# Kernel optimization log

Measured on AMD Instinct MI355X. Metric: run time of the kernel, lower is better.

Reference implementation:

```python
import jax, jax.numpy as jnp
import numpy as np

N_NODES = 50000
N_EDGES = 800000
IN_F, HID, HEADS, OUT_F = 64, 64, 4, 64
NEG_SLOPE = 0.2


def _gat_conv(x, ei, W, a_src, a_dst, b, H, C):
    """PyG-style GATConv (eval mode, add_self_loops=True, concat=True).
    x: [N, F_in], ei: [2, E], W: [F_in, H*C], a_src/a_dst: [H, C], b: [H*C].
    """
    N = x.shape[0]
    h = (x @ W).reshape(N, H, C)                      # [N,H,C]
    asrc = jnp.einsum('nhc,hc->nh', h, a_src)         # [N,H]
    adst = jnp.einsum('nhc,hc->nh', h, a_dst)         # [N,H]
    src, dst = ei[0], ei[1]
    logits = jax.nn.leaky_relu(asrc[src] + adst[dst], NEG_SLOPE)  # [E,H]
    m = jax.ops.segment_max(logits, dst, num_segments=N)
    m = jnp.where(jnp.isfinite(m), m, 0.0)
    ex = jnp.exp(logits - m[dst])
    denom = jax.ops.segment_sum(ex, dst, num_segments=N)
    alpha = ex / (denom[dst] + 1e-16)                 # [E,H]
    msg = h[src] * alpha[:, :, None]                  # [E,H,C]
    out = jax.ops.segment_sum(msg, dst, num_segments=N)  # [N,H,C]
    return out.reshape(N, H * C) + b


def _add_self_loops(ei, n):
    loops = jnp.arange(n, dtype=ei.dtype)
    return jnp.concatenate([ei, jnp.stack([loops, loops])], axis=1)


def setup_inputs() -> dict:
    key = jax.random.key(0)
    ks = jax.random.split(key, 16)
    x = jax.random.normal(ks[0], (N_NODES, IN_F), dtype=jnp.float32)
    edge_index = jax.random.randint(ks[1], (2, N_EDGES), 0, N_NODES, dtype=jnp.int32)
    s = 0.1
    d = {'x': x, 'edge_index': edge_index}
    # layer 0: IN_F -> HID, HEADS heads
    d['W0'] = jax.random.normal(ks[2], (IN_F, HEADS * HID), jnp.float32) * s
    d['a_src0'] = jax.random.normal(ks[3], (HEADS, HID), jnp.float32) * s
    d['a_dst0'] = jax.random.normal(ks[4], (HEADS, HID), jnp.float32) * s
    d['b0'] = jnp.zeros((HEADS * HID,), jnp.float32)
    # layer 1: HEADS*HID -> HID, HEADS heads
    d['W1'] = jax.random.normal(ks[5], (HEADS * HID, HEADS * HID), jnp.float32) * s
    d['a_src1'] = jax.random.normal(ks[6], (HEADS, HID), jnp.float32) * s
    d['a_dst1'] = jax.random.normal(ks[7], (HEADS, HID), jnp.float32) * s
    d['b1'] = jnp.zeros((HEADS * HID,), jnp.float32)
    # layer 2: HEADS*HID -> OUT_F, 1 head
    d['W2'] = jax.random.normal(ks[8], (HEADS * HID, OUT_F), jnp.float32) * s
    d['a_src2'] = jax.random.normal(ks[9], (1, OUT_F), jnp.float32) * s
    d['a_dst2'] = jax.random.normal(ks[10], (1, OUT_F), jnp.float32) * s
    d['b2'] = jnp.zeros((OUT_F,), jnp.float32)
    return d


def reference(x, edge_index, W0, a_src0, a_dst0, b0, W1, a_src1, a_dst1, b1, W2, a_src2, a_dst2, b2):
    ei = _add_self_loops(edge_index, x.shape[0])
    h = _gat_conv(x, ei, W0, a_src0, a_dst0, b0, HEADS, HID)
    h = jax.nn.elu(h)  # dropout identity in eval
    h = _gat_conv(h, ei, W1, a_src1, a_dst1, b1, HEADS, HID)
    h = jax.nn.elu(h)
    out = _gat_conv(h, ei, W2, a_src2, a_dst2, b2, 1, OUT_F)
    return out
```

## Files before the change

### kernel.cpp

```cpp
#include <hip/hip_runtime.h>
#include <hip/hip_fp16.h>
#include <math.h>

#define NODES 50000
#define EDGES 800000
#define NB_SCAN ((NODES + 1023) / 1024)

typedef __attribute__((ext_vector_type(8))) _Float16 f16x8;
typedef __attribute__((ext_vector_type(4))) _Float16 f16x4;
typedef __attribute__((ext_vector_type(4))) float f32x4;

__device__ __forceinline__ float lrelu02(float x){ return x > 0.f ? x : 0.2f * x; }


__global__ __launch_bounds__(256) void gat_zero(int* __restrict__ p, int n){
  int i = blockIdx.x * 256 + threadIdx.x;
  if (i < n) p[i] = 0;
}

__global__ __launch_bounds__(256) void gat_hist(const int* __restrict__ ei, int* __restrict__ cnt){
  int e = blockIdx.x * 256 + threadIdx.x;
  if (e < EDGES) atomicAdd(&cnt[ei[EDGES + e]], 1);
}

__global__ __launch_bounds__(256) void gat_blocksum(const int* __restrict__ cnt, int* __restrict__ bsums){
  __shared__ int sd[256];
  int t = threadIdx.x, b = blockIdx.x;
  int base = b * 1024 + t * 4, s = 0;
  #pragma unroll
  for (int j = 0; j < 4; j++){ int i = base + j; if (i < NODES) s += cnt[i]; }
  sd[t] = s; __syncthreads();
  for (int o = 128; o > 0; o >>= 1){ if (t < o) sd[t] += sd[t + o]; __syncthreads(); }
  if (t == 0) bsums[b] = sd[0];
}

__global__ void gat_scan_bsums(int* bsums, int nb){
  if (threadIdx.x == 0 && blockIdx.x == 0){
    int run = 0;
    for (int i = 0; i < nb; i++){ int v = bsums[i]; bsums[i] = run; run += v; }
  }
}

__global__ __launch_bounds__(256) void gat_rowptr(int* __restrict__ cnt, const int* __restrict__ bsums,
                                                  int* __restrict__ row_ptr){
  __shared__ int sd[256];
  int t = threadIdx.x, b = blockIdx.x;
  int base = b * 1024 + t * 4;
  int c[4]; int s = 0;
  #pragma unroll
  for (int j = 0; j < 4; j++){
    int i = base + j;
    c[j] = (i < NODES) ? cnt[i] : 0;
    s += c[j];
    if (i < NODES) cnt[i] = 0;
  }
  sd[t] = s; __syncthreads();
  for (int o = 1; o < 256; o <<= 1){
    int v = (t >= o) ? sd[t - o] : 0;
    __syncthreads();
    if (t >= o) sd[t] += v;
    __syncthreads();
  }
  int off = bsums[b] + sd[t] - s;
  #pragma unroll
  for (int j = 0; j < 4; j++){
    int i = base + j;
    if (i < NODES){ row_ptr[i] = off; off += c[j]; }
  }
  if (b == 0 && t == 0) row_ptr[NODES] = EDGES;
}

__global__ __launch_bounds__(256) void gat_scatter(const int* __restrict__ ei, const int* __restrict__ row_ptr,
                                                    int* __restrict__ fill, int* __restrict__ col,
                                                    int* __restrict__ dstarr){
  int e = blockIdx.x * 256 + threadIdx.x;
  if (e < EDGES){
    int s = ei[e], d = ei[EDGES + e];
    int pos = row_ptr[d] + atomicAdd(&fill[d], 1);
    col[pos] = s;
    dstarr[pos] = d;
  }
}


__global__ __launch_bounds__(256) void gat_cvt_h(const float* __restrict__ src, _Float16* __restrict__ dst, int n4){
  int i = blockIdx.x * 256 + threadIdx.x;
  if (i < n4){
    float4 v = *(const float4*)(src + (size_t)i * 4);
    f16x4 h = { (_Float16)v.x, (_Float16)v.y, (_Float16)v.z, (_Float16)v.w };
    *(f16x4*)(dst + (size_t)i * 4) = h;
  }
}

__global__ __launch_bounds__(256) void gat_wt(const float* __restrict__ W, _Float16* __restrict__ Wt, int K, int N){
  int n = blockIdx.x * 256 + threadIdx.x;
  int k = blockIdx.y;
  if (n < N) Wt[(size_t)n * K + k] = (_Float16)W[(size_t)k * N + n];
}

__global__ __launch_bounds__(256) void gat_ws0(const float* __restrict__ W0, const float* __restrict__ a_src0,
                                               const float* __restrict__ a_dst0,
                                               float* __restrict__ ws, float* __restrict__ wd){
  int t = threadIdx.x;
  int h = t >> 6, c = t & 63;
  float s = 0.f, d = 0.f;
  for (int cc = 0; cc < 64; cc++){
    float w = W0[(size_t)c * 256 + h * 64 + cc];
    s += w * a_src0[h * 64 + cc];
    d += w * a_dst0[h * 64 + cc];
  }
  ws[h * 64 + c] = s;
  wd[h * 64 + c] = d;
}


template<int K, int N>
__global__ __launch_bounds__(256) void gat_gemm_mfma(const _Float16* __restrict__ A, const _Float16* __restrict__ Wt,
                                                      _Float16* __restrict__ C, int M){
  constexpr int NT = N / 64;
  constexpr int LDT = 40;
  __shared__ _Float16 As[64][LDT];
  __shared__ _Float16 Bs[N][LDT];

  int tid = threadIdx.x;
  int w = tid >> 6, l = tid & 63;
  int lg = l >> 4, lr = l & 15;
  int bm = blockIdx.x * 64;

  f32x4 acc[4][NT];
  #pragma unroll
  for (int m = 0; m < 4; m++)
    #pragma unroll
    for (int n = 0; n < NT; n++)
      acc[m][n] = (f32x4){0.f, 0.f, 0.f, 0.f};

  int ar = tid >> 2;
  int akc = (tid & 3) * 8;
  bool avalid = (bm + ar) < M;
  const _Float16* aptr = A + (size_t)(bm + ar) * K + akc;

  for (int k0 = 0; k0 < K; k0 += 32){
    float4 av = avalid ? *(const float4*)(aptr + k0) : make_float4(0.f, 0.f, 0.f, 0.f);
    __syncthreads();
    *(float4*)&As[ar][akc] = av;
    #pragma unroll
    for (int c = 0; c < N / 64; c++){
      int idx = c * 256 + tid;
      int n = idx >> 2, kc = (idx & 3) * 8;
      *(float4*)&Bs[n][kc] = *(const float4*)(Wt + (size_t)n * K + k0 + kc);
    }
    __syncthreads();

    f16x8 af[4], bf[NT];
    #pragma unroll
    for (int m = 0; m < 4; m++) af[m] = *(const f16x8*)&As[16 * m + lr][8 * lg];
    #pragma unroll
    for (int n = 0; n < NT; n++) bf[n] = *(const f16x8*)&Bs[w * (N / 4) + 16 * n + lr][8 * lg];
    #pragma unroll
    for (int m = 0; m < 4; m++)
      #pragma unroll
      for (int n = 0; n < NT; n++)
        acc[m][n] = __builtin_amdgcn_mfma_f32_16x16x32_f16(af[m], bf[n], acc[m][n], 0, 0, 0);
  }

  #pragma unroll
  for (int m = 0; m < 4; m++){
    #pragma unroll
    for (int j = 0; j < 4; j++){
      int row = bm + 16 * m + 4 * lg + j;
      if (row < M){
        #pragma unroll
        for (int n = 0; n < NT; n++)
          C[(size_t)row * N + w * (N / 4) + 16 * n + lr] = (_Float16)acc[m][n][j];
      }
    }
  }
}


__global__ __launch_bounds__(256) void gat_gemm_bd(const _Float16* __restrict__ A, const _Float16* __restrict__ Bt,
                                                    const float* __restrict__ bias, _Float16* __restrict__ C, int M){
  int tid = threadIdx.x;
  int w = tid >> 6, l = tid & 63;
  int lg = l >> 4, lr = l & 15;
  int bm = blockIdx.x * 64;

  f32x4 acc[4][4];
  #pragma unroll
  for (int m = 0; m < 4; m++)
    #pragma unroll
    for (int n = 0; n < 4; n++)
      acc[m][n] = (f32x4){0.f, 0.f, 0.f, 0.f};

  f16x8 zf = {};
  #pragma unroll
  for (int ks = 0; ks < 2; ks++){
    int koff = ks * 32;
    f16x8 af[4], bf[4];
    #pragma unroll
    for (int m = 0; m < 4; m++){
      int row = bm + 16 * m + lr;
      af[m] = (row < M) ? *(const f16x8*)(A + (size_t)row * 256 + w * 64 + koff + 8 * lg) : zf;
    }
    #pragma unroll
    for (int n = 0; n < 4; n++)
      bf[n] = *(const f16x8*)(Bt + (size_t)(w * 64 + 16 * n + lr) * 64 + koff + 8 * lg);
    #pragma unroll
    for (int m = 0; m < 4; m++)
      #pragma unroll
      for (int n = 0; n < 4; n++)
        acc[m][n] = __builtin_amdgcn_mfma_f32_16x16x32_f16(af[m], bf[n], acc[m][n], 0, 0, 0);
  }

  #pragma unroll
  for (int m = 0; m < 4; m++){
    #pragma unroll
    for (int j = 0; j < 4; j++){
      int row = bm + 16 * m + 4 * lg + j;
      if (row < M){
        #pragma unroll
        for (int n = 0; n < 4; n++){
          int cc = w * 64 + 16 * n + lr;
          float o = acc[m][n][j] + bias[cc];
          o = o > 0.f ? o : expm1f(o);
          C[(size_t)row * 256 + cc] = (_Float16)o;
        }
      }
    }
  }
}


__global__ __launch_bounds__(256) void gat_attn0(const _Float16* __restrict__ xh, const float* __restrict__ ws,
                                                  const float* __restrict__ wd,
                                                  float* __restrict__ asrc, float* __restrict__ adst, int N){
  int lane = threadIdx.x & 63;
  int wid = threadIdx.x >> 6;
  int n = blockIdx.x * 4 + wid;
  if (n >= N) return;
  float v = (float)xh[(size_t)n * 64 + lane];
  #pragma unroll
  for (int h = 0; h < 4; h++){
    float s1 = v * ws[h * 64 + lane];
    float s2 = v * wd[h * 64 + lane];
    #pragma unroll
    for (int o = 32; o > 0; o >>= 1){ s1 += __shfl_xor(s1, o); s2 += __shfl_xor(s2, o); }
    if (lane == 0){ asrc[n * 4 + h] = s1; adst[n * 4 + h] = s2; }
  }
}

__global__ __launch_bounds__(256) void gat_attn4(const _Float16* __restrict__ h, const float* __restrict__ a_src,
                                                  const float* __restrict__ a_dst,
                                                  float* __restrict__ asrc, float* __restrict__ adst, int N){
  int lane = threadIdx.x & 63;
  int wid = threadIdx.x >> 6;
  int n = blockIdx.x * 4 + wid;
  if (n >= N) return;
  int co = lane * 4;
  f16x4 hv = *(const f16x4*)(h + (size_t)n * 256 + co);
  float4 av = *(const float4*)&a_src[co];
  float4 dv = *(const float4*)&a_dst[co];
  float f0 = (float)hv[0], f1 = (float)hv[1], f2 = (float)hv[2], f3 = (float)hv[3];
  float s1 = f0 * av.x + f1 * av.y + f2 * av.z + f3 * av.w;
  float s2 = f0 * dv.x + f1 * dv.y + f2 * dv.z + f3 * dv.w;
  #pragma unroll
  for (int o = 8; o > 0; o >>= 1){ s1 += __shfl_xor(s1, o); s2 += __shfl_xor(s2, o); }
  if ((lane & 15) == 0){
    int q = lane >> 4;
    asrc[n * 4 + q] = s1;
    adst[n * 4 + q] = s2;
  }
}

__global__ __launch_bounds__(256) void gat_attn1(const _Float16* __restrict__ h, const float* __restrict__ a_src,
                                                  const float* __restrict__ a_dst,
                                                  float* __restrict__ asrc, float* __restrict__ adst, int N){
  int lane = threadIdx.x & 63;
  int wid = threadIdx.x >> 6;
  int n = blockIdx.x * 4 + wid;
  if (n >= N) return;
  float v = (float)h[(size_t)n * 64 + lane];
  float s1 = v * a_src[lane];
  float s2 = v * a_dst[lane];
  #pragma unroll
  for (int o = 32; o > 0; o >>= 1){ s1 += __shfl_xor(s1, o); s2 += __shfl_xor(s2, o); }
  if (lane == 0){ asrc[n] = s1; adst[n] = s2; }
}


__global__ __launch_bounds__(256) void gat_edge_exp0(const int* __restrict__ col, const int* __restrict__ dstarr,
                                                      const float* __restrict__ asrc, const float* __restrict__ adst,
                                                      float* __restrict__ exf){
  int i = blockIdx.x * 256 + threadIdx.x;
  if (i >= EDGES) return;
  int s = col[i], d = dstarr[i];
  float4 a = *(const float4*)&asrc[s * 4];
  float4 b = *(const float4*)&adst[d * 4];
  float4 r;
  r.x = __expf(lrelu02(a.x + b.x));
  r.y = __expf(lrelu02(a.y + b.y));
  r.z = __expf(lrelu02(a.z + b.z));
  r.w = __expf(lrelu02(a.w + b.w));
  *(float4*)&exf[(size_t)i * 4] = r;
}


__global__ __launch_bounds__(256) void gat_aggregate_in64(const _Float16* __restrict__ xh, const float* __restrict__ exf,
                                                           const float* __restrict__ asrc, const float* __restrict__ adst,
                                                           const int* __restrict__ row_ptr, const int* __restrict__ col,
                                                           _Float16* __restrict__ agg){
  int lane = threadIdx.x & 63;
  int wid = threadIdx.x >> 6;
  int d = blockIdx.x * 4 + wid;
  if (d >= NODES) return;

  float4 ad4 = *(const float4*)&adst[d * 4];
  float4 a4  = *(const float4*)&asrc[d * 4];
  float ex0 = __expf(lrelu02(a4.x + ad4.x));
  float ex1 = __expf(lrelu02(a4.y + ad4.y));
  float ex2 = __expf(lrelu02(a4.z + ad4.z));
  float ex3 = __expf(lrelu02(a4.w + ad4.w));
  float xv = (float)xh[(size_t)d * 64 + lane];
  float acc0 = ex0 * xv, acc1 = ex1 * xv, acc2 = ex2 * xv, acc3 = ex3 * xv;
  float den0 = ex0, den1 = ex1, den2 = ex2, den3 = ex3;

  int e0 = row_ptr[d], e1 = row_ptr[d + 1];
  const _Float16* xbase = xh + lane;
  int e = e0;
  for (; e + 4 <= e1; e += 4){
    int s0 = col[e], s1 = col[e + 1], s2 = col[e + 2], s3 = col[e + 3];
    float4 fA = *(const float4*)(exf + (size_t)(e)     * 4);
    float4 fB = *(const float4*)(exf + (size_t)(e + 1) * 4);
    float4 fC = *(const float4*)(exf + (size_t)(e + 2) * 4);
    float4 fD = *(const float4*)(exf + (size_t)(e + 3) * 4);
    float v0 = (float)xbase[(size_t)s0 * 64];
    float v1 = (float)xbase[(size_t)s1 * 64];
    float v2 = (float)xbase[(size_t)s2 * 64];
    float v3 = (float)xbase[(size_t)s3 * 64];
    den0 += fA.x + fB.x + fC.x + fD.x;
    den1 += fA.y + fB.y + fC.y + fD.y;
    den2 += fA.z + fB.z + fC.z + fD.z;
    den3 += fA.w + fB.w + fC.w + fD.w;
    acc0 += fA.x * v0 + fB.x * v1 + fC.x * v2 + fD.x * v3;
    acc1 += fA.y * v0 + fB.y * v1 + fC.y * v2 + fD.y * v3;
    acc2 += fA.z * v0 + fB.z * v1 + fC.z * v2 + fD.z * v3;
    acc3 += fA.w * v0 + fB.w * v1 + fC.w * v2 + fD.w * v3;
  }
  for (; e < e1; e++){
    int s0 = col[e];
    float4 fA = *(const float4*)(exf + (size_t)e * 4);
    float v0 = (float)xbase[(size_t)s0 * 64];
    den0 += fA.x; den1 += fA.y; den2 += fA.z; den3 += fA.w;
    acc0 += fA.x * v0; acc1 += fA.y * v0; acc2 += fA.z * v0; acc3 += fA.w * v0;
  }

  _Float16* ob = agg + (size_t)d * 256 + lane;
  ob[0]   = (_Float16)(acc0 / (den0 + 1e-16f));
  ob[64]  = (_Float16)(acc1 / (den1 + 1e-16f));
  ob[128] = (_Float16)(acc2 / (den2 + 1e-16f));
  ob[192] = (_Float16)(acc3 / (den3 + 1e-16f));
}


template<bool DOELU>
__global__ __launch_bounds__(256) void gat_aggregate4(const _Float16* __restrict__ hH, const float* __restrict__ asrc,
                                                       const float* __restrict__ adst,
                                                       const int* __restrict__ row_ptr, const int* __restrict__ col,
                                                       const float* __restrict__ bias, _Float16* __restrict__ out){
  int lane = threadIdx.x & 63;
  int wid = threadIdx.x >> 6;
  int d = blockIdx.x * 4 + wid;
  if (d >= NODES) return;
  int q = lane >> 4;
  int co = lane * 4;

  float adq = adst[d * 4 + q];

  float ex = __expf(lrelu02(asrc[d * 4 + q] + adq));
  f16x4 hv = *(const f16x4*)(hH + (size_t)d * 256 + co);
  float4 acc = make_float4(ex * (float)hv[0], ex * (float)hv[1], ex * (float)hv[2], ex * (float)hv[3]);
  float den = ex;

  int e0 = row_ptr[d], e1 = row_ptr[d + 1];
  const _Float16* hbase = hH + co;
  int e = e0;
  for (; e + 4 <= e1; e += 4){
    int s0 = col[e], s1 = col[e + 1], s2 = col[e + 2], s3 = col[e + 3];
    float a0 = asrc[s0 * 4 + q], a1 = asrc[s1 * 4 + q], a2 = asrc[s2 * 4 + q], a3 = asrc[s3 * 4 + q];
    f16x4 h0 = *(const f16x4*)(hbase + (size_t)s0 * 256);
    f16x4 h1 = *(const f16x4*)(hbase + (size_t)s1 * 256);
    f16x4 h2 = *(const f16x4*)(hbase + (size_t)s2 * 256);
    f16x4 h3 = *(const f16x4*)(hbase + (size_t)s3 * 256);
    float x0 = __expf(lrelu02(a0 + adq));
    float x1 = __expf(lrelu02(a1 + adq));
    float x2 = __expf(lrelu02(a2 + adq));
    float x3 = __expf(lrelu02(a3 + adq));
    den += x0 + x1 + x2 + x3;
    acc.x += x0 * (float)h0[0] + x1 * (float)h1[0] + x2 * (float)h2[0] + x3 * (float)h3[0];
    acc.y += x0 * (float)h0[1] + x1 * (float)h1[1] + x2 * (float)h2[1] + x3 * (float)h3[1];
    acc.z += x0 * (float)h0[2] + x1 * (float)h1[2] + x2 * (float)h2[2] + x3 * (float)h3[2];
    acc.w += x0 * (float)h0[3] + x1 * (float)h1[3] + x2 * (float)h2[3] + x3 * (float)h3[3];
  }
  for (; e < e1; e++){
    int s0 = col[e];
    float a0 = asrc[s0 * 4 + q];
    f16x4 h0 = *(const f16x4*)(hbase + (size_t)s0 * 256);
    float x0 = __expf(lrelu02(a0 + adq));
    den += x0;
    acc.x += x0 * (float)h0[0]; acc.y += x0 * (float)h0[1];
    acc.z += x0 * (float)h0[2]; acc.w += x0 * (float)h0[3];
  }

  float inv = 1.f / (den + 1e-16f);
  float4 b4 = *(const float4*)&bias[co];
  float4 o = make_float4(acc.x * inv + b4.x, acc.y * inv + b4.y, acc.z * inv + b4.z, acc.w * inv + b4.w);
  if (DOELU){
    o.x = o.x > 0.f ? o.x : expm1f(o.x);
    o.y = o.y > 0.f ? o.y : expm1f(o.y);
    o.z = o.z > 0.f ? o.z : expm1f(o.z);
    o.w = o.w > 0.f ? o.w : expm1f(o.w);
  }
  f16x4 oh = { (_Float16)o.x, (_Float16)o.y, (_Float16)o.z, (_Float16)o.w };
  *(f16x4*)(out + (size_t)d * 256 + co) = oh;
}

__global__ __launch_bounds__(256) void gat_aggregate1(const _Float16* __restrict__ hH, const float* __restrict__ asrc,
                                                       const float* __restrict__ adst,
                                                       const int* __restrict__ row_ptr, const int* __restrict__ col,
                                                       const float* __restrict__ bias, float* __restrict__ out){
  int lane = threadIdx.x & 63;
  int wid = threadIdx.x >> 6;
  int d = blockIdx.x * 4 + wid;
  if (d >= NODES) return;

  float adq = adst[d];
  float ex = __expf(lrelu02(asrc[d] + adq));
  float acc = ex * (float)hH[(size_t)d * 64 + lane];
  float den = ex;

  int e0 = row_ptr[d], e1 = row_ptr[d + 1];
  const _Float16* hbase = hH + lane;
  int e = e0;
  for (; e + 4 <= e1; e += 4){
    int s0 = col[e], s1 = col[e + 1], s2 = col[e + 2], s3 = col[e + 3];
    float a0 = asrc[s0], a1 = asrc[s1], a2 = asrc[s2], a3 = asrc[s3];
    float v0 = (float)hbase[(size_t)s0 * 64];
    float v1 = (float)hbase[(size_t)s1 * 64];
    float v2 = (float)hbase[(size_t)s2 * 64];
    float v3 = (float)hbase[(size_t)s3 * 64];
    float x0 = __expf(lrelu02(a0 + adq));
    float x1 = __expf(lrelu02(a1 + adq));
    float x2 = __expf(lrelu02(a2 + adq));
    float x3 = __expf(lrelu02(a3 + adq));
    den += x0 + x1 + x2 + x3;
    acc += x0 * v0 + x1 * v1 + x2 * v2 + x3 * v3;
  }
  for (; e < e1; e++){
    int s0 = col[e];
    float x0 = __expf(lrelu02(asrc[s0] + adq));
    den += x0;
    acc += x0 * (float)hbase[(size_t)s0 * 64];
  }
  out[(size_t)d * 64 + lane] = acc / (den + 1e-16f) + bias[lane];
}


extern "C" void kernel_launch(void* const* d_in, const int* in_sizes, int n_in,
                              void* d_out, int out_size, void* d_ws, size_t ws_size,
                              hipStream_t stream) {
  const float* x   = (const float*)d_in[0];
  const int*   ei  = (const int*)  d_in[1];
  const float* W0  = (const float*)d_in[2];
  const float* as0 = (const float*)d_in[3];
  const float* ad0 = (const float*)d_in[4];
  const float* b0  = (const float*)d_in[5];
  const float* W1  = (const float*)d_in[6];
  const float* as1 = (const float*)d_in[7];
  const float* ad1 = (const float*)d_in[8];
  const float* b1  = (const float*)d_in[9];
  const float* W2  = (const float*)d_in[10];
  const float* as2 = (const float*)d_in[11];
  const float* ad2 = (const float*)d_in[12];
  const float* b2  = (const float*)d_in[13];
  float* out = (float*)d_out;

  auto al = [](size_t v){ return (v + 255) & ~(size_t)255; };
  char* p = (char*)d_ws;
  int*      row_ptr = (int*)p;      p += al((NODES + 1) * sizeof(int));
  int*      cnt     = (int*)p;      p += al(NODES * sizeof(int));
  int*      bsums   = (int*)p;      p += al(64 * sizeof(int));
  int*      col     = (int*)p;      p += al(EDGES * sizeof(int));
  int*      dstarr  = (int*)p;      p += al(EDGES * sizeof(int));
  float*    exf     = (float*)p;    p += al((size_t)EDGES * 4 * sizeof(float));
  float*    asrc    = (float*)p;    p += al(NODES * 4 * sizeof(float));
  float*    adst    = (float*)p;    p += al(NODES * 4 * sizeof(float));
  _Float16* xh      = (_Float16*)p; p += al((size_t)NODES * 64 * sizeof(_Float16));
  _Float16* hH      = (_Float16*)p; p += al((size_t)NODES * 256 * sizeof(_Float16));
  _Float16* actb    = (_Float16*)p; p += al((size_t)NODES * 256 * sizeof(_Float16));
  _Float16* Wt0     = (_Float16*)p; p += al(256 * 64 * sizeof(_Float16));
  _Float16* Wt1     = (_Float16*)p; p += al(256 * 256 * sizeof(_Float16));
  _Float16* Wt2     = (_Float16*)p; p += al(64 * 256 * sizeof(_Float16));
  float*    ws0     = (float*)p;    p += al(256 * sizeof(float));
  float*    wd0     = (float*)p;    p += al(256 * sizeof(float));

  gat_cvt_h<<<(NODES * 64 / 4 + 255) / 256, 256, 0, stream>>>(x, xh, NODES * 64 / 4);
  gat_wt<<<dim3(1, 64), 256, 0, stream>>>(W0, Wt0, 64, 256);
  gat_wt<<<dim3(1, 256), 256, 0, stream>>>(W1, Wt1, 256, 256);
  gat_wt<<<dim3(1, 256), 256, 0, stream>>>(W2, Wt2, 256, 64);
  gat_ws0<<<1, 256, 0, stream>>>(W0, as0, ad0, ws0, wd0);

  gat_zero<<<(NODES + 255) / 256, 256, 0, stream>>>(cnt, NODES);
  gat_hist<<<(EDGES + 255) / 256, 256, 0, stream>>>(ei, cnt);
  gat_blocksum<<<NB_SCAN, 256, 0, stream>>>(cnt, bsums);
  gat_scan_bsums<<<1, 64, 0, stream>>>(bsums, NB_SCAN);
  gat_rowptr<<<NB_SCAN, 256, 0, stream>>>(cnt, bsums, row_ptr);
  gat_scatter<<<(EDGES + 255) / 256, 256, 0, stream>>>(ei, row_ptr, cnt, col, dstarr);

  const int nodeBlocks = (NODES + 3) / 4;
  const int gemmBlocks = (NODES + 63) / 64;
  const int edgeBlocks = (EDGES + 255) / 256;

  gat_attn0<<<nodeBlocks, 256, 0, stream>>>(xh, ws0, wd0, asrc, adst, NODES);
  gat_edge_exp0<<<edgeBlocks, 256, 0, stream>>>(col, dstarr, asrc, adst, exf);
  gat_aggregate_in64<<<nodeBlocks, 256, 0, stream>>>(xh, exf, asrc, adst, row_ptr, col, hH);
  gat_gemm_bd<<<gemmBlocks, 256, 0, stream>>>(hH, Wt0, b0, actb, NODES);

  gat_gemm_mfma<256, 256><<<gemmBlocks, 256, 0, stream>>>(actb, Wt1, hH, NODES);
  gat_attn4<<<nodeBlocks, 256, 0, stream>>>(hH, as1, ad1, asrc, adst, NODES);
  gat_aggregate4<true><<<nodeBlocks, 256, 0, stream>>>(hH, asrc, adst, row_ptr, col, b1, actb);

  gat_gemm_mfma<256, 64><<<gemmBlocks, 256, 0, stream>>>(actb, Wt2, hH, NODES);
  gat_attn1<<<nodeBlocks, 256, 0, stream>>>(hH, as2, ad2, asrc, adst, NODES);
  gat_aggregate1<<<nodeBlocks, 256, 0, stream>>>(hH, asrc, adst, row_ptr, col, b2, out);
}
```

Before: 377.9 us.

## Split edges across lane slots in aggregations, precompute layer-2 exps, merge weight transposes

The layer-0 and layer-2 aggregation kernels now have each wavefront process four edges at a time, with 16 lanes per edge loading vectorized f16x4 features and reducing across slots with xor shuffles. A new edge-parallel kernel precomputes the layer-2 attention exponentials. The layer-1 aggregation now peels to 4-edge alignment and unrolls by 8 using int4 column loads. The three weight-transpose launches are merged into one. The aim is more memory-level parallelism on the gathers and fewer launches, at the cost of extra shuffles and one additional edge pass.

```diff
diff --git a/kernel.cpp b/kernel.cpp
--- a/kernel.cpp
+++ b/kernel.cpp
@@ -11,6 +11,13 @@
 typedef __attribute__((ext_vector_type(4))) float f32x4;
 
 __device__ __forceinline__ float lrelu02(float x){ return x > 0.f ? x : 0.2f * x; }
+
+__device__ __forceinline__ f32x4 shflx4(f32x4 v, int m){
+  f32x4 r;
+  r[0] = __shfl_xor(v[0], m); r[1] = __shfl_xor(v[1], m);
+  r[2] = __shfl_xor(v[2], m); r[3] = __shfl_xor(v[3], m);
+  return r;
+}
 
 
 __global__ __launch_bounds__(256) void gat_zero(int* __restrict__ p, int n){
@@ -92,10 +99,21 @@
   }
 }
 
-__global__ __launch_bounds__(256) void gat_wt(const float* __restrict__ W, _Float16* __restrict__ Wt, int K, int N){
-  int n = blockIdx.x * 256 + threadIdx.x;
-  int k = blockIdx.y;
-  if (n < N) Wt[(size_t)n * K + k] = (_Float16)W[(size_t)k * N + n];
+__global__ __launch_bounds__(256) void gat_wt_all(const float* __restrict__ W0, const float* __restrict__ W1,
+                                                  const float* __restrict__ W2,
+                                                  _Float16* __restrict__ Wt0, _Float16* __restrict__ Wt1,
+                                                  _Float16* __restrict__ Wt2){
+  int n = threadIdx.x;
+  int k = blockIdx.x;
+  if (k < 64){
+    Wt0[(size_t)n * 64 + k] = (_Float16)W0[(size_t)k * 256 + n];
+  } else if (k < 320){
+    int kk = k - 64;
+    Wt1[(size_t)n * 256 + kk] = (_Float16)W1[(size_t)kk * 256 + n];
+  } else {
+    int kk = k - 320;
+    if (n < 64) Wt2[(size_t)n * 256 + kk] = (_Float16)W2[(size_t)kk * 64 + n];
+  }
 }
 
 __global__ __launch_bounds__(256) void gat_ws0(const float* __restrict__ W0, const float* __restrict__ a_src0,
@@ -304,6 +322,14 @@
   *(float4*)&exf[(size_t)i * 4] = r;
 }
 
+__global__ __launch_bounds__(256) void gat_edge_exp1h(const int* __restrict__ col, const int* __restrict__ dstarr,
+                                                       const float* __restrict__ asrc, const float* __restrict__ adst,
+                                                       float* __restrict__ exf1){
+  int i = blockIdx.x * 256 + threadIdx.x;
+  if (i >= EDGES) return;
+  exf1[i] = __expf(lrelu02(asrc[col[i]] + adst[dstarr[i]]));
+}
+
 
 __global__ __launch_bounds__(256) void gat_aggregate_in64(const _Float16* __restrict__ xh, const float* __restrict__ exf,
                                                            const float* __restrict__ asrc, const float* __restrict__ adst,
@@ -313,56 +339,88 @@
   int wid = threadIdx.x >> 6;
   int d = blockIdx.x * 4 + wid;
   if (d >= NODES) return;
-
-  float4 ad4 = *(const float4*)&adst[d * 4];
-  float4 a4  = *(const float4*)&asrc[d * 4];
-  float ex0 = __expf(lrelu02(a4.x + ad4.x));
-  float ex1 = __expf(lrelu02(a4.y + ad4.y));
-  float ex2 = __expf(lrelu02(a4.z + ad4.z));
-  float ex3 = __expf(lrelu02(a4.w + ad4.w));
-  float xv = (float)xh[(size_t)d * 64 + lane];
-  float acc0 = ex0 * xv, acc1 = ex1 * xv, acc2 = ex2 * xv, acc3 = ex3 * xv;
-  float den0 = ex0, den1 = ex1, den2 = ex2, den3 = ex3;
+  int slot = lane >> 4;
+  int cpos = (lane & 15) * 4;
+
+  f32x4 acc0 = {0,0,0,0}, acc1 = {0,0,0,0}, acc2 = {0,0,0,0}, acc3 = {0,0,0,0};
+  f32x4 den = {0,0,0,0};
 
   int e0 = row_ptr[d], e1 = row_ptr[d + 1];
-  const _Float16* xbase = xh + lane;
+  const _Float16* xb = xh + cpos;
   int e = e0;
-  for (; e + 4 <= e1; e += 4){
-    int s0 = col[e], s1 = col[e + 1], s2 = col[e + 2], s3 = col[e + 3];
-    float4 fA = *(const float4*)(exf + (size_t)(e)     * 4);
-    float4 fB = *(const float4*)(exf + (size_t)(e + 1) * 4);
-    float4 fC = *(const float4*)(exf + (size_t)(e + 2) * 4);
-    float4 fD = *(const float4*)(exf + (size_t)(e + 3) * 4);
-    float v0 = (float)xbase[(size_t)s0 * 64];
-    float v1 = (float)xbase[(size_t)s1 * 64];
-    float v2 = (float)xbase[(size_t)s2 * 64];
-    float v3 = (float)xbase[(size_t)s3 * 64];
-    den0 += fA.x + fB.x + fC.x + fD.x;
-    den1 += fA.y + fB.y + fC.y + fD.y;
-    den2 += fA.z + fB.z + fC.z + fD.z;
-    den3 += fA.w + fB.w + fC.w + fD.w;
-    acc0 += fA.x * v0 + fB.x * v1 + fC.x * v2 + fD.x * v3;
-    acc1 += fA.y * v0 + fB.y * v1 + fC.y * v2 + fD.y * v3;
-    acc2 += fA.z * v0 + fB.z * v1 + fC.z * v2 + fD.z * v3;
-    acc3 += fA.w * v0 + fB.w * v1 + fC.w * v2 + fD.w * v3;
-  }
-  for (; e < e1; e++){
-    int s0 = col[e];
-    float4 fA = *(const float4*)(exf + (size_t)e * 4);
-    float v0 = (float)xbase[(size_t)s0 * 64];
-    den0 += fA.x; den1 += fA.y; den2 += fA.z; den3 += fA.w;
-    acc0 += fA.x * v0; acc1 += fA.y * v0; acc2 += fA.z * v0; acc3 += fA.w * v0;
-  }
-
-  _Float16* ob = agg + (size_t)d * 256 + lane;
-  ob[0]   = (_Float16)(acc0 / (den0 + 1e-16f));
-  ob[64]  = (_Float16)(acc1 / (den1 + 1e-16f));
-  ob[128] = (_Float16)(acc2 / (den2 + 1e-16f));
-  ob[192] = (_Float16)(acc3 / (den3 + 1e-16f));
-}
-
-
-template<bool DOELU>
+  for (; e + 8 <= e1; e += 8){
+    int eA = e + slot, eB = e + 4 + slot;
+    int sA = col[eA], sB = col[eB];
+    float4 fA = *(const float4*)(exf + (size_t)eA * 4);
+    float4 fB = *(const float4*)(exf + (size_t)eB * 4);
+    f16x4 hA = *(const f16x4*)(xb + (size_t)sA * 64);
+    f16x4 hB = *(const f16x4*)(xb + (size_t)sB * 64);
+    f32x4 vA = { (float)hA[0], (float)hA[1], (float)hA[2], (float)hA[3] };
+    f32x4 vB = { (float)hB[0], (float)hB[1], (float)hB[2], (float)hB[3] };
+    den += (f32x4){ fA.x + fB.x, fA.y + fB.y, fA.z + fB.z, fA.w + fB.w };
+    acc0 += fA.x * vA + fB.x * vB;
+    acc1 += fA.y * vA + fB.y * vB;
+    acc2 += fA.z * vA + fB.z * vB;
+    acc3 += fA.w * vA + fB.w * vB;
+  }
+  if (e + 4 <= e1){
+    int eA = e + slot;
+    int sA = col[eA];
+    float4 fA = *(const float4*)(exf + (size_t)eA * 4);
+    f16x4 hA = *(const f16x4*)(xb + (size_t)sA * 64);
+    f32x4 vA = { (float)hA[0], (float)hA[1], (float)hA[2], (float)hA[3] };
+    den += (f32x4){ fA.x, fA.y, fA.z, fA.w };
+    acc0 += fA.x * vA; acc1 += fA.y * vA; acc2 += fA.z * vA; acc3 += fA.w * vA;
+    e += 4;
+  }
+  {
+    int eA = e + slot;
+    if (eA < e1){
+      int sA = col[eA];
+      float4 fA = *(const float4*)(exf + (size_t)eA * 4);
+      f16x4 hA = *(const f16x4*)(xb + (size_t)sA * 64);
+      f32x4 vA = { (float)hA[0], (float)hA[1], (float)hA[2], (float)hA[3] };
+      den += (f32x4){ fA.x, fA.y, fA.z, fA.w };
+      acc0 += fA.x * vA; acc1 += fA.y * vA; acc2 += fA.z * vA; acc3 += fA.w * vA;
+    }
+  }
+
+  #pragma unroll
+  for (int off = 16; off <= 32; off <<= 1){
+    acc0 += shflx4(acc0, off);
+    acc1 += shflx4(acc1, off);
+    acc2 += shflx4(acc2, off);
+    acc3 += shflx4(acc3, off);
+    den  += shflx4(den,  off);
+  }
+
+  float4 a4 = *(const float4*)&asrc[d * 4];
+  float4 b4 = *(const float4*)&adst[d * 4];
+  float es0 = __expf(lrelu02(a4.x + b4.x));
+  float es1 = __expf(lrelu02(a4.y + b4.y));
+  float es2 = __expf(lrelu02(a4.z + b4.z));
+  float es3 = __expf(lrelu02(a4.w + b4.w));
+  f16x4 hs = *(const f16x4*)(xh + (size_t)d * 64 + cpos);
+  f32x4 vs = { (float)hs[0], (float)hs[1], (float)hs[2], (float)hs[3] };
+  acc0 += es0 * vs; acc1 += es1 * vs; acc2 += es2 * vs; acc3 += es3 * vs;
+  den += (f32x4){ es0, es1, es2, es3 };
+
+  if (slot == 0){
+    float i0 = 1.f / (den[0] + 1e-16f), i1 = 1.f / (den[1] + 1e-16f);
+    float i2 = 1.f / (den[2] + 1e-16f), i3 = 1.f / (den[3] + 1e-16f);
+    _Float16* ob = agg + (size_t)d * 256 + cpos;
+    f16x4 o0 = { (_Float16)(acc0[0]*i0), (_Float16)(acc0[1]*i0), (_Float16)(acc0[2]*i0), (_Float16)(acc0[3]*i0) };
+    f16x4 o1 = { (_Float16)(acc1[0]*i1), (_Float16)(acc1[1]*i1), (_Float16)(acc1[2]*i1), (_Float16)(acc1[3]*i1) };
+    f16x4 o2 = { (_Float16)(acc2[0]*i2), (_Float16)(acc2[1]*i2), (_Float16)(acc2[2]*i2), (_Float16)(acc2[3]*i2) };
+    f16x4 o3 = { (_Float16)(acc3[0]*i3), (_Float16)(acc3[1]*i3), (_Float16)(acc3[2]*i3), (_Float16)(acc3[3]*i3) };
+    *(f16x4*)(ob)       = o0;
+    *(f16x4*)(ob + 64)  = o1;
+    *(f16x4*)(ob + 128) = o2;
+    *(f16x4*)(ob + 192) = o3;
+  }
+}
+
+
 __global__ __launch_bounds__(256) void gat_aggregate4(const _Float16* __restrict__ hH, const float* __restrict__ asrc,
                                                        const float* __restrict__ adst,
                                                        const int* __restrict__ row_ptr, const int* __restrict__ col,
@@ -384,22 +442,41 @@
   int e0 = row_ptr[d], e1 = row_ptr[d + 1];
   const _Float16* hbase = hH + co;
   int e = e0;
-  for (; e + 4 <= e1; e += 4){
-    int s0 = col[e], s1 = col[e + 1], s2 = col[e + 2], s3 = col[e + 3];
-    float a0 = asrc[s0 * 4 + q], a1 = asrc[s1 * 4 + q], a2 = asrc[s2 * 4 + q], a3 = asrc[s3 * 4 + q];
+  for (; e < e1 && (e & 3); e++){
+    int s0 = col[e];
+    float a0 = asrc[s0 * 4 + q];
     f16x4 h0 = *(const f16x4*)(hbase + (size_t)s0 * 256);
-    f16x4 h1 = *(const f16x4*)(hbase + (size_t)s1 * 256);
-    f16x4 h2 = *(const f16x4*)(hbase + (size_t)s2 * 256);
-    f16x4 h3 = *(const f16x4*)(hbase + (size_t)s3 * 256);
     float x0 = __expf(lrelu02(a0 + adq));
-    float x1 = __expf(lrelu02(a1 + adq));
-    float x2 = __expf(lrelu02(a2 + adq));
-    float x3 = __expf(lrelu02(a3 + adq));
-    den += x0 + x1 + x2 + x3;
-    acc.x += x0 * (float)h0[0] + x1 * (float)h1[0] + x2 * (float)h2[0] + x3 * (float)h3[0];
-    acc.y += x0 * (float)h0[1] + x1 * (float)h1[1] + x2 * (float)h2[1] + x3 * (float)h3[1];
-    acc.z += x0 * (float)h0[2] + x1 * (float)h1[2] + x2 * (float)h2[2] + x3 * (float)h3[2];
-    acc.w += x0 * (float)h0[3] + x1 * (float)h1[3] + x2 * (float)h2[3] + x3 * (float)h3[3];
+    den += x0;
+    acc.x += x0 * (float)h0[0]; acc.y += x0 * (float)h0[1];
+    acc.z += x0 * (float)h0[2]; acc.w += x0 * (float)h0[3];
+  }
+  for (; e + 8 <= e1; e += 8){
+    int4 cA = *(const int4*)&col[e];
+    int4 cB = *(const int4*)&col[e + 4];
+    float a0 = asrc[cA.x * 4 + q], a1 = asrc[cA.y * 4 + q], a2 = asrc[cA.z * 4 + q], a3 = asrc[cA.w * 4 + q];
+    float a4 = asrc[cB.x * 4 + q], a5 = asrc[cB.y * 4 + q], a6 = asrc[cB.z * 4 + q], a7 = asrc[cB.w * 4 + q];
+    f16x4 h0 = *(const f16x4*)(hbase + (size_t)cA.x * 256);
+    f16x4 h1 = *(const f16x4*)(hbase + (size_t)cA.y * 256);
+    f16x4 h2 = *(const f16x4*)(hbase + (size_t)cA.z * 256);
+    f16x4 h3 = *(const f16x4*)(hbase + (size_t)cA.w * 256);
+    f16x4 h4 = *(const f16x4*)(hbase + (size_t)cB.x * 256);
+    f16x4 h5 = *(const f16x4*)(hbase + (size_t)cB.y * 256);
+    f16x4 h6 = *(const f16x4*)(hbase + (size_t)cB.z * 256);
+    f16x4 h7 = *(const f16x4*)(hbase + (size_t)cB.w * 256);
+    float x0 = __expf(lrelu02(a0 + adq)), x1 = __expf(lrelu02(a1 + adq));
+    float x2 = __expf(lrelu02(a2 + adq)), x3 = __expf(lrelu02(a3 + adq));
+    float x4 = __expf(lrelu02(a4 + adq)), x5 = __expf(lrelu02(a5 + adq));
+    float x6 = __expf(lrelu02(a6 + adq)), x7 = __expf(lrelu02(a7 + adq));
+    den += x0 + x1 + x2 + x3 + x4 + x5 + x6 + x7;
+    acc.x += x0 * (float)h0[0] + x1 * (float)h1[0] + x2 * (float)h2[0] + x3 * (float)h3[0]
+           + x4 * (float)h4[0] + x5 * (float)h5[0] + x6 * (float)h6[0] + x7 * (float)h7[0];
+    acc.y += x0 * (float)h0[1] + x1 * (float)h1[1] + x2 * (float)h2[1] + x3 * (float)h3[1]
+           + x4 * (float)h4[1] + x5 * (float)h5[1] + x6 * (float)h6[1] + x7 * (float)h7[1];
+    acc.z += x0 * (float)h0[2] + x1 * (float)h1[2] + x2 * (float)h2[2] + x3 * (float)h3[2]
+           + x4 * (float)h4[2] + x5 * (float)h5[2] + x6 * (float)h6[2] + x7 * (float)h7[2];
+    acc.w += x0 * (float)h0[3] + x1 * (float)h1[3] + x2 * (float)h2[3] + x3 * (float)h3[3]
+           + x4 * (float)h4[3] + x5 * (float)h5[3] + x6 * (float)h6[3] + x7 * (float)h7[3];
   }
   for (; e < e1; e++){
     int s0 = col[e];
@@ -414,54 +491,81 @@
   float inv = 1.f / (den + 1e-16f);
   float4 b4 = *(const float4*)&bias[co];
   float4 o = make_float4(acc.x * inv + b4.x, acc.y * inv + b4.y, acc.z * inv + b4.z, acc.w * inv + b4.w);
-  if (DOELU){
-    o.x = o.x > 0.f ? o.x : expm1f(o.x);
-    o.y = o.y > 0.f ? o.y : expm1f(o.y);
-    o.z = o.z > 0.f ? o.z : expm1f(o.z);
-    o.w = o.w > 0.f ? o.w : expm1f(o.w);
-  }
+  o.x = o.x > 0.f ? o.x : expm1f(o.x);
+  o.y = o.y > 0.f ? o.y : expm1f(o.y);
+  o.z = o.z > 0.f ? o.z : expm1f(o.z);
+  o.w = o.w > 0.f ? o.w : expm1f(o.w);
   f16x4 oh = { (_Float16)o.x, (_Float16)o.y, (_Float16)o.z, (_Float16)o.w };
   *(f16x4*)(out + (size_t)d * 256 + co) = oh;
 }
 
-__global__ __launch_bounds__(256) void gat_aggregate1(const _Float16* __restrict__ hH, const float* __restrict__ asrc,
-                                                       const float* __restrict__ adst,
-                                                       const int* __restrict__ row_ptr, const int* __restrict__ col,
-                                                       const float* __restrict__ bias, float* __restrict__ out){
+
+__global__ __launch_bounds__(256) void gat_aggregate1n(const _Float16* __restrict__ hH, const float* __restrict__ exf1,
+                                                        const float* __restrict__ asrc, const float* __restrict__ adst,
+                                                        const int* __restrict__ row_ptr, const int* __restrict__ col,
+                                                        const float* __restrict__ bias, float* __restrict__ out){
   int lane = threadIdx.x & 63;
   int wid = threadIdx.x >> 6;
   int d = blockIdx.x * 4 + wid;
   if (d >= NODES) return;
-
-  float adq = adst[d];
-  float ex = __expf(lrelu02(asrc[d] + adq));
-  float acc = ex * (float)hH[(size_t)d * 64 + lane];
-  float den = ex;
+  int slot = lane >> 4;
+  int cpos = (lane & 15) * 4;
+
+  f32x4 acc = {0,0,0,0};
+  float den = 0.f;
 
   int e0 = row_ptr[d], e1 = row_ptr[d + 1];
-  const _Float16* hbase = hH + lane;
+  const _Float16* hb = hH + cpos;
   int e = e0;
-  for (; e + 4 <= e1; e += 4){
-    int s0 = col[e], s1 = col[e + 1], s2 = col[e + 2], s3 = col[e + 3];
-    float a0 = asrc[s0], a1 = asrc[s1], a2 = asrc[s2], a3 = asrc[s3];
-    float v0 = (float)hbase[(size_t)s0 * 64];
-    float v1 = (float)hbase[(size_t)s1 * 64];
-    float v2 = (float)hbase[(size_t)s2 * 64];
-    float v3 = (float)hbase[(size_t)s3 * 64];
-    float x0 = __expf(lrelu02(a0 + adq));
-    float x1 = __expf(lrelu02(a1 + adq));
-    float x2 = __expf(lrelu02(a2 + adq));
-    float x3 = __expf(lrelu02(a3 + adq));
-    den += x0 + x1 + x2 + x3;
-    acc += x0 * v0 + x1 * v1 + x2 * v2 + x3 * v3;
-  }
-  for (; e < e1; e++){
-    int s0 = col[e];
-    float x0 = __expf(lrelu02(asrc[s0] + adq));
-    den += x0;
-    acc += x0 * (float)hbase[(size_t)s0 * 64];
-  }
-  out[(size_t)d * 64 + lane] = acc / (den + 1e-16f) + bias[lane];
+  for (; e + 8 <= e1; e += 8){
+    int eA = e + slot, eB = e + 4 + slot;
+    int sA = col[eA], sB = col[eB];
+    float fA = exf1[eA], fB = exf1[eB];
+    f16x4 hA = *(const f16x4*)(hb + (size_t)sA * 64);
+    f16x4 hB = *(const f16x4*)(hb + (size_t)sB * 64);
+    f32x4 vA = { (float)hA[0], (float)hA[1], (float)hA[2], (float)hA[3] };
+    f32x4 vB = { (float)hB[0], (float)hB[1], (float)hB[2], (float)hB[3] };
+    den += fA + fB;
+    acc += fA * vA + fB * vB;
+  }
+  if (e + 4 <= e1){
+    int eA = e + slot;
+    int sA = col[eA];
+    float fA = exf1[eA];
+    f16x4 hA = *(const f16x4*)(hb + (size_t)sA * 64);
+    f32x4 vA = { (float)hA[0], (float)hA[1], (float)hA[2], (float)hA[3] };
+    den += fA; acc += fA * vA;
+    e += 4;
+  }
+  {
+    int eA = e + slot;
+    if (eA < e1){
+      int sA = col[eA];
+      float fA = exf1[eA];
+      f16x4 hA = *(const f16x4*)(hb + (size_t)sA * 64);
+      f32x4 vA = { (float)hA[0], (float)hA[1], (float)hA[2], (float)hA[3] };
+      den += fA; acc += fA * vA;
+    }
+  }
+
+  #pragma unroll
+  for (int off = 16; off <= 32; off <<= 1){
+    acc += shflx4(acc, off);
+    den += __shfl_xor(den, off);
+  }
+
+  float es = __expf(lrelu02(asrc[d] + adst[d]));
+  f16x4 hs = *(const f16x4*)(hH + (size_t)d * 64 + cpos);
+  f32x4 vs = { (float)hs[0], (float)hs[1], (float)hs[2], (float)hs[3] };
+  acc += es * vs;
+  den += es;
+
+  if (slot == 0){
+    float inv = 1.f / (den + 1e-16f);
+    float4 b4 = *(const float4*)&bias[cpos];
+    float4 o = make_float4(acc[0] * inv + b4.x, acc[1] * inv + b4.y, acc[2] * inv + b4.z, acc[3] * inv + b4.w);
+    *(float4*)(out + (size_t)d * 64 + cpos) = o;
+  }
 }
 
 
@@ -504,9 +608,7 @@
   float*    wd0     = (float*)p;    p += al(256 * sizeof(float));
 
   gat_cvt_h<<<(NODES * 64 / 4 + 255) / 256, 256, 0, stream>>>(x, xh, NODES * 64 / 4);
-  gat_wt<<<dim3(1, 64), 256, 0, stream>>>(W0, Wt0, 64, 256);
-  gat_wt<<<dim3(1, 256), 256, 0, stream>>>(W1, Wt1, 256, 256);
-  gat_wt<<<dim3(1, 256), 256, 0, stream>>>(W2, Wt2, 256, 64);
+  gat_wt_all<<<576, 256, 0, stream>>>(W0, W1, W2, Wt0, Wt1, Wt2);
   gat_ws0<<<1, 256, 0, stream>>>(W0, as0, ad0, ws0, wd0);
 
   gat_zero<<<(NODES + 255) / 256, 256, 0, stream>>>(cnt, NODES);
@@ -527,9 +629,10 @@
 
   gat_gemm_mfma<256, 256><<<gemmBlocks, 256, 0, stream>>>(actb, Wt1, hH, NODES);
   gat_attn4<<<nodeBlocks, 256, 0, stream>>>(hH, as1, ad1, asrc, adst, NODES);
-  gat_aggregate4<true><<<nodeBlocks, 256, 0, stream>>>(hH, asrc, adst, row_ptr, col, b1, actb);
+  gat_aggregate4<<<nodeBlocks, 256, 0, stream>>>(hH, asrc, adst, row_ptr, col, b1, actb);
 
   gat_gemm_mfma<256, 64><<<gemmBlocks, 256, 0, stream>>>(actb, Wt2, hH, NODES);
   gat_attn1<<<nodeBlocks, 256, 0, stream>>>(hH, as2, ad2, asrc, adst, NODES);
-  gat_aggregate1<<<nodeBlocks, 256, 0, stream>>>(hH, asrc, adst, row_ptr, col, b2, out);
-}
+  gat_edge_exp1h<<<edgeBlocks, 256, 0, stream>>>(col, dstarr, asrc, adst, exf);
+  gat_aggregate1n<<<nodeBlocks, 256, 0, stream>>>(hH, exf, asrc, adst, row_ptr, col, b2, out);
+}
```

Measured after the change: 373.4 us. About the same (-1.2%).
